# Kernel optimization log

Measured on AMD Instinct MI355X. Metric: run time of the kernel, lower is better.

## Reference

```python
import jax, jax.numpy as jnp
import numpy as np

KERNEL_SIZE = 11
OUT_CH = 512
IN_CH = 512


def make_pos_grid(k):
    # centered integer offsets, grid flattened at the end: shape (2, k*k)
    coords = jnp.arange(k, dtype=jnp.float32) - (k - 1) / 2.0
    yy, xx = jnp.meshgrid(coords, coords, indexing="ij")
    return jnp.stack([yy.reshape(-1), xx.reshape(-1)], axis=0)  # (2, k*k)


def setup_inputs() -> dict:
    key = jax.random.key(0)
    k1, _ = jax.random.split(key)
    # raw Cholesky parameters per (out_channel, in_channel) pair; diagonal goes
    # through exp() in reference() to guarantee positive-definite covariances.
    chol_raw = 0.1 * jax.random.normal(k1, (OUT_CH, IN_CH, 2, 2), dtype=jnp.float32)
    pos_grid = make_pos_grid(KERNEL_SIZE)
    return {"chol_raw": chol_raw, "pos_grid": pos_grid}


def reference(chol_raw, pos_grid):
    # chol_raw: (O, I, 2, 2) raw params; pos_grid: (2, K) with K = k*k
    O, I = chol_raw.shape[0], chol_raw.shape[1]
    K = pos_grid.shape[-1]
    k = int(round(np.sqrt(K)))

    # Lower-triangular Cholesky factor with positive diagonal:
    # L = [[exp(a), 0], [c, exp(d)]]
    l11 = jnp.exp(chol_raw[..., 0, 0])[..., None]  # (O, I, 1)
    l21 = chol_raw[..., 1, 0][..., None]           # (O, I, 1)
    l22 = jnp.exp(chol_raw[..., 1, 1])[..., None]  # (O, I, 1)

    x1 = pos_grid[0]  # (K,)
    x2 = pos_grid[1]  # (K,)

    # Inlined forward substitution: solve L b = x for each (o, i, position)
    b1 = x1 / l11                    # (O, I, K)
    b2 = (x2 - l21 * b1) / l22       # (O, I, K)

    # dists = sum over the 2-vector of squares = x^T S^{-1} x
    dists = (b1 * b1 + b2 * b2).reshape((O, I, k, k))
    return dists
```

## Files before the change

kernel.cpp:

```cpp
#include <hip/hip_runtime.h>

#define KK 121
#define NPAIR (512 * 512)
#define PPB 64
#define NBLK (NPAIR / PPB)
#define F4PB (PPB * KK / 4)

typedef float floatx4 __attribute__((ext_vector_type(4)));

__global__ __launch_bounds__(256, 8) void
quad_stream_kernel(const float4* __restrict__ chol4,
                   const float* __restrict__ pg,
                   float4* __restrict__ out4) {
    __shared__ float4 s_pqr[PPB];
    __shared__ float4 s_uvw[KK];

    const int t = threadIdx.x;

    if (t < KK) {
        float x1 = pg[t];
        float x2 = pg[KK + t];
        s_uvw[t] = make_float4(x1 * x1, x2 * x2, x1 * x2, 0.f);
    }
    if (t < PPB) {
        float4 c = chol4[blockIdx.x * PPB + t];
        float e1 = __expf(-c.x);
        float e2 = __expf(-c.w);
        float f  = c.z * e2;
        float P  = e1 * e1 * fmaf(f, f, 1.f);
        float Q  = e2 * e2;
        float R  = -2.f * f * e1 * e2;
        s_pqr[t] = make_float4(P, Q, R, 0.f);
    }
    __syncthreads();

    floatx4* o = (floatx4*)(out4 + (size_t)blockIdx.x * F4PB);
#pragma unroll 2
    for (int i = t; i < F4PB; i += 256) {
        const int f0 = 4 * i;
        floatx4 res;
#pragma unroll
        for (int e = 0; e < 4; ++e) {
            const int fe = f0 + e;
            const int p  = (fe * 17333) >> 21;
            const int k  = fe - 121 * p;
            const float4 pqr = s_pqr[p];
            const float4 uvw = s_uvw[k];
            res[e] = fmaf(pqr.x, uvw.x, fmaf(pqr.y, uvw.y, pqr.z * uvw.z));
        }
        __builtin_nontemporal_store(res, &o[i]);
    }
}

extern "C" void kernel_launch(void* const* d_in, const int* in_sizes, int n_in,
                              void* d_out, int out_size, void* d_ws, size_t ws_size,
                              hipStream_t stream) {
    const float4* chol4 = (const float4*)d_in[0];
    const float* pg     = (const float*)d_in[1];
    float4* out4        = (float4*)d_out;

    quad_stream_kernel<<<NBLK, 256, 0, stream>>>(chol4, pg, out4);
}
```

Baseline: 152.2 us.

## Map lanes to kernel positions and loop over pairs per wave

Reorganizes the output loop so each lane owns fixed grid positions (k and k+64) held in registers, and each wave iterates over its 16 pairs. This removes the per-element division-by-121 index math and the per-element LDS lookups of both tables. The cost is that stores become scalar 4-byte writes without the nontemporal hint, at misaligned row offsets. The 57-lane tail also leaves some lanes idle on the second store.

```diff
diff --git a/kernel.cpp b/kernel.cpp
--- a/kernel.cpp
+++ b/kernel.cpp
@@ -4,14 +4,12 @@
 #define NPAIR (512 * 512)
 #define PPB 64
 #define NBLK (NPAIR / PPB)
-#define F4PB (PPB * KK / 4)
-
-typedef float floatx4 __attribute__((ext_vector_type(4)));
+#define PAIRS_PER_WAVE (PPB / 4)
 
 __global__ __launch_bounds__(256, 8) void
-quad_stream_kernel(const float4* __restrict__ chol4,
-                   const float* __restrict__ pg,
-                   float4* __restrict__ out4) {
+quad_lanek_kernel(const float4* __restrict__ chol4,
+                  const float* __restrict__ pg,
+                  float* __restrict__ out) {
     __shared__ float4 s_pqr[PPB];
     __shared__ float4 s_uvw[KK];
 
@@ -34,21 +32,25 @@
     }
     __syncthreads();
 
-    floatx4* o = (floatx4*)(out4 + (size_t)blockIdx.x * F4PB);
-#pragma unroll 2
-    for (int i = t; i < F4PB; i += 256) {
-        const int f0 = 4 * i;
-        floatx4 res;
+    const int lane = t & 63;
+    const int wave = t >> 6;
+    const bool hasB = (lane < KK - 64);
+
+    const float4 uvwA = s_uvw[lane];
+    const float4 uvwB = s_uvw[hasB ? (64 + lane) : lane];
+
+    float* ob = out + (size_t)blockIdx.x * (PPB * KK);
+
 #pragma unroll
-        for (int e = 0; e < 4; ++e) {
-            const int fe = f0 + e;
-            const int p  = (fe * 17333) >> 21;
-            const int k  = fe - 121 * p;
-            const float4 pqr = s_pqr[p];
-            const float4 uvw = s_uvw[k];
-            res[e] = fmaf(pqr.x, uvw.x, fmaf(pqr.y, uvw.y, pqr.z * uvw.z));
+    for (int j = 0; j < PAIRS_PER_WAVE; ++j) {
+        const int p = wave * PAIRS_PER_WAVE + j;
+        const float4 c = s_pqr[p];
+        const float rA = fmaf(c.x, uvwA.x, fmaf(c.y, uvwA.y, c.z * uvwA.z));
+        ob[p * KK + lane] = rA;
+        if (hasB) {
+            const float rB = fmaf(c.x, uvwB.x, fmaf(c.y, uvwB.y, c.z * uvwB.z));
+            ob[p * KK + 64 + lane] = rB;
         }
-        __builtin_nontemporal_store(res, &o[i]);
     }
 }
 
@@ -57,7 +59,7 @@
                               hipStream_t stream) {
     const float4* chol4 = (const float4*)d_in[0];
     const float* pg     = (const float*)d_in[1];
-    float4* out4        = (float4*)d_out;
+    float* out          = (float*)d_out;
 
-    quad_stream_kernel<<<NBLK, 256, 0, stream>>>(chol4, pg, out4);
+    quad_lanek_kernel<<<NBLK, 256, 0, stream>>>(chol4, pg, out);
 }
```

After: 131.3 us. 13.7% less time.
